# Kernel optimization log

Hardware: AMD Instinct MI355X
Metric: run time of the kernel (lower is better)

Reference implementation:

```python
import jax, jax.numpy as jnp
import numpy as np

D_MODEL = 1024
B, S = 4, 2048


def setup_inputs() -> dict:
    key = jax.random.key(0)
    kx, km, kq, kk, kv, ko = jax.random.split(key, 6)
    x = jax.random.normal(kx, (B, S, D_MODEL), dtype=jnp.float32)
    mask = jax.random.randint(km, (B, S, S), 0, 2).astype(jnp.bool_)
    # flax Dense default kernel init: lecun_normal-ish; plain scaled normal is fine for a reference
    init_scale = 1.0 / np.sqrt(D_MODEL)
    Wq = jax.random.normal(kq, (D_MODEL, D_MODEL), dtype=jnp.float32) * init_scale
    Wk = jax.random.normal(kk, (D_MODEL, D_MODEL), dtype=jnp.float32) * init_scale
    Wv = jax.random.normal(kv, (D_MODEL, D_MODEL), dtype=jnp.float32) * init_scale
    Wo = jax.random.normal(ko, (D_MODEL, D_MODEL), dtype=jnp.float32) * init_scale
    return {"x": x, "mask": mask, "Wq": Wq, "Wk": Wk, "Wv": Wv, "Wo": Wo}


def reference(x, mask, Wq, Wk, Wv, Wo):
    # QKV projections (use_bias=False)
    q = jnp.einsum('bsd,de->bse', x, Wq)
    k = jnp.einsum('bsd,de->bse', x, Wk)
    v = jnp.einsum('bsd,de->bse', x, Wv)
    scale = jnp.sqrt(jnp.asarray(q.shape[-1], x.dtype)).astype(x.dtype)
    # [B, S, S] attention scores
    attn_scores = jnp.einsum('bqd,bkd->bqk', q, k) / scale
    attn_scores = jnp.where(mask, attn_scores, jnp.asarray(-1e10, x.dtype))
    attn_weights = jax.nn.softmax(attn_scores, axis=-1)
    attn_output = jnp.einsum('bqk,bkd->bqd', attn_weights, v)
    return jnp.einsum('bsd,de->bse', attn_output, Wo)
```

## Files before the change

### kernel.cpp

```cpp
#include <hip/hip_runtime.h>


#define DM 1024
#define SQ 2048
#define NB 4
typedef unsigned short U16;
typedef short bhalf8 __attribute__((ext_vector_type(8)));
typedef float f32x4 __attribute__((ext_vector_type(4)));

__device__ inline U16 f2bf(float f) {
  unsigned int u = __float_as_uint(f);
  u += 0x7FFFu + ((u >> 16) & 1u);
  return (U16)(u >> 16);
}
__device__ inline float2 bfp2(unsigned int u) {
  float2 r;
  r.x = __uint_as_float(u << 16);
  r.y = __uint_as_float(u & 0xffff0000u);
  return r;
}
__device__ inline unsigned int packbf(float a, float b) {
  return (unsigned int)f2bf(a) | ((unsigned int)f2bf(b) << 16);
}

__device__ __forceinline__ void gload16(const U16* g, const U16* l) {
  unsigned int m0v =
      (unsigned int)__builtin_amdgcn_readfirstlane((int)(unsigned long long)l);
  asm volatile("s_mov_b32 m0, %0\n\t"
               "global_load_lds_dwordx4 %1, off"
               :
               : "s"(m0v), "v"(g)
               : "memory");
}

__global__ __launch_bounds__(256) void conv_f32_bf16(
    const float* __restrict__ src, U16* __restrict__ dst, float* __restrict__ rs) {
  int idx = blockIdx.x * 256 + threadIdx.x;
  if (idx < NB * SQ) rs[idx] = 0.f;
  int i = idx * 8;
  float4 a = *(const float4*)(src + i);
  float4 b = *(const float4*)(src + i + 4);
  uint4 w;
  w.x = packbf(a.x, a.y); w.y = packbf(a.z, a.w);
  w.z = packbf(b.x, b.y); w.w = packbf(b.z, b.w);
  *(uint4*)(dst + i) = w;
}

__device__ inline void ldcvt16(const float* p, U16* d) {
#pragma unroll
  for (int i = 0; i < 4; ++i) {
    float4 f = *(const float4*)(p + i * 4);
    d[i * 4 + 0] = f2bf(f.x); d[i * 4 + 1] = f2bf(f.y);
    d[i * 4 + 2] = f2bf(f.z); d[i * 4 + 3] = f2bf(f.w);
  }
}
__device__ inline void ldcvt16(const U16* p, U16* d) {
  uint4 a = *(const uint4*)p;
  uint4 b = *(const uint4*)(p + 8);
  *(uint4*)d = a;
  *(uint4*)(d + 8) = b;
}

__global__ __launch_bounds__(256) void transp_w4(
    const float* __restrict__ Wq, const float* __restrict__ Wk,
    const float* __restrict__ Wo, const float* __restrict__ Wv,
    U16* __restrict__ WT, U16* __restrict__ WoT, U16* __restrict__ Wv16) {
  __shared__ U16 tile[64][72];
  const int z = blockIdx.z;
  const int r0 = blockIdx.y * 64, c0 = blockIdx.x * 64;
  const int t = threadIdx.x;
  const int tr = t >> 2, tc = (t & 3) * 16;
  if (z == 3) {
    U16 vals[16];
    ldcvt16(Wv + (size_t)(r0 + tr) * DM + c0 + tc, vals);
    U16* op = Wv16 + (size_t)(r0 + tr) * DM + c0 + tc;
    *(uint4*)op = *(uint4*)&vals[0];
    *(uint4*)(op + 8) = *(uint4*)&vals[8];
    return;
  }
  const float* src = (z == 0) ? Wq : (z == 1) ? Wk : Wo;
  U16* d = (z == 2) ? WoT : WT + (size_t)z * DM * DM;
  ldcvt16(src + (size_t)(r0 + tr) * DM + c0 + tc, &tile[tr][tc]);
  __syncthreads();
  U16 vals[16];
#pragma unroll
  for (int m = 0; m < 16; ++m) vals[m] = tile[tc + m][tr];
  U16* op = d + (size_t)(c0 + tr) * DM + r0 + tc;
  *(uint4*)op = *(uint4*)&vals[0];
  *(uint4*)(op + 8) = *(uint4*)&vals[8];
}

__global__ __launch_bounds__(256) void transp_bf16(
    const U16* __restrict__ src, U16* __restrict__ dst, int R, int C) {
  __shared__ U16 tile[64][72];
  const int z = blockIdx.z;
  src += (size_t)z * R * C;
  dst += (size_t)z * R * C;
  const int r0 = blockIdx.y * 64, c0 = blockIdx.x * 64;
  const int t = threadIdx.x;
  const int tr = t >> 2, tc = (t & 3) * 16;
  ldcvt16(src + (size_t)(r0 + tr) * C + c0 + tc, &tile[tr][tc]);
  __syncthreads();
  U16 vals[16];
#pragma unroll
  for (int m = 0; m < 16; ++m) vals[m] = tile[tc + m][tr];
  U16* op = dst + (size_t)(c0 + tr) * R + r0 + tc;
  *(uint4*)op = *(uint4*)&vals[0];
  *(uint4*)(op + 8) = *(uint4*)&vals[8];
}

template <int EP>
__global__ __launch_bounds__(256) void gemm_mfma(
    const U16* __restrict__ A, const U16* __restrict__ B, void* __restrict__ Cv,
    int M, int N, int K, long long sA, long long sB, long long sC,
    const int* __restrict__ mask, float* __restrict__ rowsum, float scale) {
  __shared__ U16 As[128 * 72];
  __shared__ U16 Bs[128 * 72];
  const int t = threadIdx.x;
  const int lane = t & 63, wave = t >> 6;
  const int wm = wave >> 1, wn = wave & 1;
  const int q = lane >> 4, ln = lane & 15;
  const int z = blockIdx.z;
  const int m0 = blockIdx.y * 128, n0 = blockIdx.x * 128;
  A += (size_t)z * sA;
  B += (size_t)z * sB;

  f32x4 acc[4][4] = {};

  const int srow = t >> 3;
  const int scol = (t & 7) * 8;

  for (int k0 = 0; k0 < K; k0 += 64) {
    const U16* ga = A + (size_t)(m0 + srow) * K + k0 + scol;
    const U16* gb = B + (size_t)(n0 + srow) * K + k0 + scol;
#pragma unroll
    for (int it = 0; it < 4; ++it) {
      uint4 va = *(const uint4*)(ga + (size_t)it * 32 * K);
      uint4 vb = *(const uint4*)(gb + (size_t)it * 32 * K);
      *(uint4*)&As[(it * 32 + srow) * 72 + scol] = va;
      *(uint4*)&Bs[(it * 32 + srow) * 72 + scol] = vb;
    }
    __syncthreads();
#pragma unroll
    for (int kk = 0; kk < 64; kk += 32) {
      bhalf8 af[4], bg[4];
#pragma unroll
      for (int i = 0; i < 4; ++i) {
        af[i] = *(const bhalf8*)&As[(wm * 64 + i * 16 + ln) * 72 + kk + q * 8];
        bg[i] = *(const bhalf8*)&Bs[(wn * 64 + i * 16 + ln) * 72 + kk + q * 8];
      }
#pragma unroll
      for (int i = 0; i < 4; ++i)
#pragma unroll
        for (int j = 0; j < 4; ++j)
          acc[i][j] = __builtin_amdgcn_mfma_f32_16x16x32_bf16(af[i], bg[j], acc[i][j], 0, 0, 0);
    }
    __syncthreads();
  }

#pragma unroll
  for (int i = 0; i < 4; ++i) {
#pragma unroll
    for (int r = 0; r < 4; ++r) {
      const int rr = m0 + wm * 64 + i * 16 + q * 4 + r;
      float linv = 0.f;
      if constexpr (EP == 2) linv = 1.0f / (rowsum[(size_t)z * M + rr] + 1e-30f);
      float psum = 0.f;
#pragma unroll
      for (int j = 0; j < 4; ++j) {
        const int c = n0 + wn * 64 + j * 16 + ln;
        float v = acc[i][j][r];
        if constexpr (EP == 0) {
          ((U16*)Cv)[(size_t)z * sC + (size_t)rr * N + c] = f2bf(v);
        } else if constexpr (EP == 1) {
          int mk = mask[((size_t)z * M + rr) * N + c];
          float p = mk ? __expf(v * scale) : 0.f;
          U16 pb = f2bf(p);
          ((U16*)Cv)[(size_t)z * sC + (size_t)rr * N + c] = pb;
          psum += __uint_as_float((unsigned int)pb << 16);
        } else {
          ((float*)Cv)[(size_t)z * sC + (size_t)rr * N + c] = v * linv;
        }
      }
      if constexpr (EP == 1) {
#pragma unroll
        for (int off = 8; off > 0; off >>= 1) psum += __shfl_xor(psum, off, 64);
        if (ln == 0) atomicAdd(&rowsum[(size_t)z * M + rr], psum);
      }
    }
  }
}

template <int EP, int WM>
__global__ __launch_bounds__(512, 1) void gemm8(
    const U16* __restrict__ A, const U16* __restrict__ B, void* __restrict__ Cv,
    int M, int N, int K, long long sA, long long sB, long long sC,
    const int* __restrict__ mask, float* __restrict__ rowsum, float scale) {
  constexpr int WN = 8 / WM;
  constexpr int BN = WN * 64;
  constexpr int MR = 256 / WM;
  constexpr int FM = MR / 16;
  constexpr int IMq = FM / 2;
  constexpr int HB = BN / 2;
  constexpr int CB = HB / 64;
  constexpr int VW = 4 + 2 * CB;
  __shared__ __attribute__((aligned(16))) U16 Abuf[2][256 * 64];
  __shared__ __attribute__((aligned(16))) U16 Bbuf[2][BN * 64];
  const int t = threadIdx.x;
  const int lane = t & 63, wave = t >> 6;
  const int wm = wave / WN, wn = wave % WN;
  const int q = lane >> 4, ln = lane & 15;
  const int lxor = ln & 7;
  const int z = blockIdx.z;
  const int m0 = blockIdx.y * 256, n0 = blockIdx.x * BN;
  const U16* Abase = A + (size_t)z * sA + (size_t)m0 * K;
  const U16* Bbase = B + (size_t)z * sB + (size_t)n0 * K;

  const int pr = wave * 8 + (lane >> 3);
  const int cchunk = (((lane & 7) ^ ((lane >> 3) & 7)) << 3);
  int la[4];
#pragma unroll
  for (int c = 0; c < 4; ++c) {
    int p = c * 64 + pr;
    int mh = p >> 7, q64 = p & 127;
    la[c] = (q64 / (MR / 2)) * MR + mh * (MR / 2) + (q64 % (MR / 2));
  }
  int lb[4] = {0, 0, 0, 0};
#pragma unroll
  for (int c = 0; c < 2 * CB; ++c) {
    int p = c * 64 + pr;
    int nh = p / HB, rem = p % HB;
    lb[c] = (rem >> 5) * 64 + nh * 32 + (rem & 31);
  }
  const U16* gA0 = Abase + (size_t)la[0] * K + cchunk;
  const U16* gA1 = Abase + (size_t)la[1] * K + cchunk;
  const U16* gA2 = Abase + (size_t)la[2] * K + cchunk;
  const U16* gA3 = Abase + (size_t)la[3] * K + cchunk;
  const U16* gB0 = Bbase + (size_t)lb[0] * K + cchunk;
  const U16* gB1 = (CB == 2) ? Bbase + (size_t)lb[1] * K + cchunk : gB0;
  const U16* gB2 = Bbase + (size_t)lb[CB] * K + cchunk;
  const U16* gB3 = (CB == 2) ? Bbase + (size_t)lb[3] * K + cchunk : gB2;
  const int wofs = wave * 8 * 64;

#define ST_AX(bi, ko) { gload16(gA0 + (ko), &Abuf[bi][0 * 64 + wofs]);         \
                        gload16(gA1 + (ko), &Abuf[bi][64 * 64 + wofs]); }
#define ST_AY(bi, ko) { gload16(gA2 + (ko), &Abuf[bi][128 * 64 + wofs]);       \
                        gload16(gA3 + (ko), &Abuf[bi][192 * 64 + wofs]); }
#define ST_BE(bi, ko) { gload16(gB0 + (ko), &Bbuf[bi][0 * 64 + wofs]);         \
                        if (CB == 2) gload16(gB1 + (ko), &Bbuf[bi][64 * 64 + wofs]); }
#define ST_BO(bi, ko) { gload16(gB2 + (ko), &Bbuf[bi][HB * 64 + wofs]);        \
                        if (CB == 2) gload16(gB3 + (ko), &Bbuf[bi][(HB + 64) * 64 + wofs]); }

  f32x4 acc[FM][4] = {};
  bhalf8 af[IMq][2], bgE[2][2], bgO[2][2];

#define LDA(bi, mh) {                                                          \
  _Pragma("unroll") for (int im = 0; im < IMq; ++im)                           \
  _Pragma("unroll") for (int kx = 0; kx < 2; ++kx)                             \
    af[im][kx] = *(const bhalf8*)&Abuf[bi][                                    \
        ((mh) * 128 + wm * (MR / 2) + im * 16 + ln) * 64 +                     \
        (((kx * 4 + q) ^ lxor) << 3)]; }
#define LDB(bi, nh, BG) {                                                      \
  _Pragma("unroll") for (int jn = 0; jn < 2; ++jn)                             \
  _Pragma("unroll") for (int kx = 0; kx < 2; ++kx)                             \
    BG[jn][kx] = *(const bhalf8*)&Bbuf[bi][                                    \
        ((nh) * HB + wn * 32 + jn * 16 + ln) * 64 +                            \
        (((kx * 4 + q) ^ lxor) << 3)]; }
#define MQ(mh, nh, BG) {                                                       \
  __builtin_amdgcn_s_setprio(1);                                               \
  _Pragma("unroll") for (int im = 0; im < IMq; ++im)                           \
  _Pragma("unroll") for (int jn = 0; jn < 2; ++jn)                             \
  _Pragma("unroll") for (int kx = 0; kx < 2; ++kx)                             \
    acc[(mh) * IMq + im][(nh) * 2 + jn] =                                      \
        __builtin_amdgcn_mfma_f32_16x16x32_bf16(                               \
            af[im][kx], BG[jn][kx], acc[(mh) * IMq + im][(nh) * 2 + jn],       \
            0, 0, 0);                                                          \
  __builtin_amdgcn_s_setprio(0); }
#define WAITV(n) asm volatile("s_waitcnt vmcnt(%0)" :: "i"(n) : "memory")
#define BAR() __builtin_amdgcn_s_barrier()
#define LGKM0() asm volatile("s_waitcnt lgkmcnt(0)" ::: "memory")

#define TILE8(bi, nbi, kA, kB)                                                 \
  {                                                                            \
    ST_BO(nbi, kA); WAITV(VW);                                                 \
    LDA(bi, 0); LDB(bi, 0, bgE);                                               \
    BAR(); LGKM0(); MQ(0, 0, bgE); BAR();                                      \
    ST_AY(nbi, kA); WAITV(VW);                                                 \
    LDB(bi, 1, bgO);                                                           \
    BAR(); LGKM0(); MQ(0, 1, bgO); BAR();                                      \
    ST_AX(bi, kB); WAITV(VW);                                                  \
    LDA(bi, 1);                                                                \
    BAR(); LGKM0(); MQ(1, 0, bgE); BAR();                                      \
    ST_BE(bi, kB); WAITV(VW);                                                  \
    BAR(); LGKM0(); MQ(1, 1, bgO); BAR();                                      \
  }

  const int NT = K >> 6;
  ST_AX(0, 0); ST_BE(0, 0); ST_BO(0, 0); ST_AY(0, 0);
  ST_AX(1, 64); ST_BE(1, 64);
  WAITV(VW); BAR();
  for (int tt = 0; tt < NT; tt += 2) {
    const int k1 = (tt + 1) * 64;
    const int k2 = (tt + 2 < NT) ? (tt + 2) * 64 : 0;
    const int k3 = (tt + 3 < NT) ? (tt + 3) * 64 : 0;
    TILE8(0, 1, k1, k2);
    TILE8(1, 0, k2, k3);
  }
  WAITV(0);

#undef ST_AX
#undef ST_AY
#undef ST_BE
#undef ST_BO
#undef LDA
#undef LDB
#undef MQ
#undef WAITV
#undef BAR
#undef LGKM0
#undef TILE8

#pragma unroll
  for (int i = 0; i < FM; ++i) {
#pragma unroll
    for (int r = 0; r < 4; ++r) {
      const int rr = m0 + wm * MR + i * 16 + q * 4 + r;
      float linv = 0.f;
      if constexpr (EP == 2) linv = 1.0f / (rowsum[(size_t)z * M + rr] + 1e-30f);
      float psum = 0.f;
#pragma unroll
      for (int j = 0; j < 4; ++j) {
        const int c = n0 + wn * 64 + j * 16 + ln;
        float v = acc[i][j][r];
        if constexpr (EP == 0) {
          ((U16*)Cv)[(size_t)z * sC + (size_t)rr * N + c] = f2bf(v);
        } else if constexpr (EP == 1) {
          int mk = mask[((size_t)z * M + rr) * N + c];
          float p = mk ? __expf(v * scale) : 0.f;
          U16 pb = f2bf(p);
          ((U16*)Cv)[(size_t)z * sC + (size_t)rr * N + c] = pb;
          psum += __uint_as_float((unsigned int)pb << 16);
        } else {
          ((float*)Cv)[(size_t)z * sC + (size_t)rr * N + c] = v * linv;
        }
      }
      if constexpr (EP == 1) {
#pragma unroll
        for (int off = 8; off > 0; off >>= 1) psum += __shfl_xor(psum, off, 64);
        if (ln == 0) atomicAdd(&rowsum[(size_t)z * M + rr], psum);
      }
    }
  }
}

__device__ inline float4 load4(const float* p) { return *(const float4*)p; }
__device__ inline float4 load4(const U16* p) {
  uint2 w = *(const uint2*)p;
  float2 f0 = bfp2(w.x), f1 = bfp2(w.y);
  return make_float4(f0.x, f0.y, f1.x, f1.y);
}
__device__ inline void store4(float* p, float a, float b, float c, float d) {
  *(float4*)p = make_float4(a, b, c, d);
}
__device__ inline void store4(U16* p, float a, float b, float c, float d) {
  uint2 w;
  w.x = packbf(a, b);
  w.y = packbf(c, d);
  *(uint2*)p = w;
}
template <typename TA, typename TB, typename TC>
__global__ __launch_bounds__(256) void gemm_t(
    const TA* __restrict__ A, const TB* __restrict__ B,
    TC* __restrict__ C, int M, int N, int K) {
  __shared__ float As[16][64];
  __shared__ float Bs[16][64];
  const int t = threadIdx.x;
  const int tx = t & 15, ty = t >> 4;
  const int m0 = blockIdx.y * 64;
  const int n0 = blockIdx.x * 64;
  const int arow = t >> 2, akq = (t & 3) * 4;
  const int brow = t >> 4, bcg = (t & 15) * 4;
  float acc[4][4] = {};
  for (int k0 = 0; k0 < K; k0 += 16) {
    {
      float4 f = load4(A + (size_t)(m0 + arow) * K + k0 + akq);
      As[akq + 0][arow] = f.x; As[akq + 1][arow] = f.y;
      As[akq + 2][arow] = f.z; As[akq + 3][arow] = f.w;
    }
    {
      float4 f = load4(B + (size_t)(k0 + brow) * N + n0 + bcg);
      *(float4*)&Bs[brow][bcg] = f;
    }
    __syncthreads();
#pragma unroll
    for (int kk = 0; kk < 16; ++kk) {
      float4 a = *(const float4*)&As[kk][ty * 4];
      float4 b = *(const float4*)&Bs[kk][tx * 4];
      float av[4] = {a.x, a.y, a.z, a.w};
      float bv[4] = {b.x, b.y, b.z, b.w};
#pragma unroll
      for (int i = 0; i < 4; ++i)
#pragma unroll
        for (int j = 0; j < 4; ++j) acc[i][j] += av[i] * bv[j];
    }
    __syncthreads();
  }
#pragma unroll
  for (int i = 0; i < 4; ++i)
    store4(&C[(size_t)(m0 + ty * 4 + i) * N + n0 + tx * 4],
           acc[i][0], acc[i][1], acc[i][2], acc[i][3]);
}
__global__ __launch_bounds__(256) void flash_wave(
    const U16* __restrict__ Q, const U16* __restrict__ Kd,
    const U16* __restrict__ V, const int* __restrict__ mask,
    U16* __restrict__ O) {
  __shared__ float q_s[4][DM];
  const int t = threadIdx.x;
  const int w = t >> 6;
  const int lane = t & 63;
  const int row = blockIdx.x * 4 + w;
  const int b = row >> 11;
  const size_t bo = (size_t)b * SQ * DM;
  const size_t mrow0 = (size_t)row * SQ;
  {
    const U16* qp = Q + (size_t)row * DM + lane * 16;
    uint4 w0 = *(const uint4*)qp;
    uint4 w1 = *(const uint4*)(qp + 8);
    float* dst = &q_s[w][lane * 16];
    float2 f;
    f = bfp2(w0.x); dst[0] = f.x;  dst[1] = f.y;
    f = bfp2(w0.y); dst[2] = f.x;  dst[3] = f.y;
    f = bfp2(w0.z); dst[4] = f.x;  dst[5] = f.y;
    f = bfp2(w0.w); dst[6] = f.x;  dst[7] = f.y;
    f = bfp2(w1.x); dst[8] = f.x;  dst[9] = f.y;
    f = bfp2(w1.y); dst[10] = f.x; dst[11] = f.y;
    f = bfp2(w1.z); dst[12] = f.x; dst[13] = f.y;
    f = bfp2(w1.w); dst[14] = f.x; dst[15] = f.y;
  }
  __syncthreads();
  float m = -3.0e38f, l = 0.f;
  float o[16] = {};
  const int dbase = lane * 16;
  const float* qrow = q_s[w];
  for (int j0 = 0; j0 < SQ; j0 += 64) {
    float s;
    {
      const U16* kp = Kd + bo + (size_t)(j0 + lane) * DM;
      float acc = 0.f;
      for (int d = 0; d < DM; d += 8) {
        uint4 kw = *(const uint4*)(kp + d);
        float2 a0 = bfp2(kw.x), a1 = bfp2(kw.y), a2 = bfp2(kw.z), a3 = bfp2(kw.w);
        acc += qrow[d] * a0.x + qrow[d + 1] * a0.y + qrow[d + 2] * a1.x +
               qrow[d + 3] * a1.y + qrow[d + 4] * a2.x + qrow[d + 5] * a2.y +
               qrow[d + 6] * a3.x + qrow[d + 7] * a3.y;
      }
      s = acc * 0.03125f;
      if (mask[mrow0 + j0 + lane] == 0) s = -1e10f;
    }
    float ms = s;
#pragma unroll
    for (int off = 32; off > 0; off >>= 1) ms = fmaxf(ms, __shfl_xor(ms, off, 64));
    float mn = fmaxf(m, ms);
    float alpha = __expf(m - mn);
    float p = __expf(s - mn);
    float ps = p;
#pragma unroll
    for (int off = 32; off > 0; off >>= 1) ps += __shfl_xor(ps, off, 64);
    l = l * alpha + ps;
    m = mn;
#pragma unroll
    for (int k = 0; k < 16; ++k) o[k] *= alpha;
    const U16* vp = V + bo + (size_t)j0 * DM + dbase;
    for (int j = 0; j < 64; ++j) {
      float pj = __shfl(p, j, 64);
      uint4 v0 = *(const uint4*)(vp + (size_t)j * DM);
      uint4 v1 = *(const uint4*)(vp + (size_t)j * DM + 8);
      float2 f0 = bfp2(v0.x), f1 = bfp2(v0.y), f2 = bfp2(v0.z), f3 = bfp2(v0.w);
      float2 g0 = bfp2(v1.x), g1 = bfp2(v1.y), g2 = bfp2(v1.z), g3 = bfp2(v1.w);
      o[0] += pj * f0.x;  o[1] += pj * f0.y;  o[2] += pj * f1.x;  o[3] += pj * f1.y;
      o[4] += pj * f2.x;  o[5] += pj * f2.y;  o[6] += pj * f3.x;  o[7] += pj * f3.y;
      o[8] += pj * g0.x;  o[9] += pj * g0.y;  o[10] += pj * g1.x; o[11] += pj * g1.y;
      o[12] += pj * g2.x; o[13] += pj * g2.y; o[14] += pj * g3.x; o[15] += pj * g3.y;
    }
  }
  float linv = (l > 0.f) ? (1.0f / l) : 0.f;
  U16* op = O + (size_t)row * DM + dbase;
  uint4 r0, r1;
  r0.x = packbf(o[0] * linv, o[1] * linv);
  r0.y = packbf(o[2] * linv, o[3] * linv);
  r0.z = packbf(o[4] * linv, o[5] * linv);
  r0.w = packbf(o[6] * linv, o[7] * linv);
  r1.x = packbf(o[8] * linv, o[9] * linv);
  r1.y = packbf(o[10] * linv, o[11] * linv);
  r1.z = packbf(o[12] * linv, o[13] * linv);
  r1.w = packbf(o[14] * linv, o[15] * linv);
  *(uint4*)op = r0;
  *(uint4*)(op + 8) = r1;
}

extern "C" void kernel_launch(void* const* d_in, const int* in_sizes, int n_in,
                              void* d_out, int out_size, void* d_ws, size_t ws_size,
                              hipStream_t stream) {
  const float* x  = (const float*)d_in[0];
  const int* mask = (const int*)d_in[1];
  const float* Wq = (const float*)d_in[2];
  const float* Wk = (const float*)d_in[3];
  const float* Wv = (const float*)d_in[4];
  const float* Wo = (const float*)d_in[5];
  float* out = (float*)d_out;

  const size_t MB = 1u << 20;
  const size_t E = (size_t)NB * SQ * DM;
  const size_t WE = (size_t)DM * DM;

  if (ws_size >= 121 * MB) {
    char* ws = (char*)d_ws;
    U16* WT   = (U16*)ws;
    U16* WoT  = (U16*)(ws + 6 * MB);
    U16* x16  = (U16*)(ws + 8 * MB);
    U16* Q16  = (U16*)(ws + 24 * MB);
    U16* K16  = (U16*)(ws + 40 * MB);
    U16* U16b = (U16*)(ws + 56 * MB);
    U16* Wv16 = (U16*)(ws + 72 * MB);
    U16* UT16 = (U16*)(ws + 72 * MB);
    U16* P16  = (U16*)(ws + 88 * MB);
    float* rs = (float*)(ws + 120 * MB);

    conv_f32_bf16<<<dim3(E / (256 * 8)), 256, 0, stream>>>(x, x16, rs);
    transp_w4<<<dim3(16, 16, 4), 256, 0, stream>>>(Wq, Wk, Wo, Wv, WT, WoT, Wv16);

    gemm_mfma<0><<<dim3(DM / 128, DM / 128, 1), 256, 0, stream>>>(
        WoT, Wv16, WT + 2 * WE, DM, DM, DM, 0, 0, 0, nullptr, nullptr, 0.f);

    gemm8<0, 4><<<dim3(DM / 128, (NB * SQ) / 256, 3), 512, 0, stream>>>(
        x16, WT, Q16, NB * SQ, DM, DM,
        0, (long long)WE, (long long)E, nullptr, nullptr, 0.f);

    transp_bf16<<<dim3(DM / 64, SQ / 64, NB), 256, 0, stream>>>(U16b, UT16, SQ, DM);

    gemm8<1, 2><<<dim3(SQ / 256, SQ / 256, NB), 512, 0, stream>>>(
        Q16, K16, P16, SQ, SQ, DM,
        (long long)SQ * DM, (long long)SQ * DM, (long long)SQ * SQ,
        mask, rs, 0.03125f);

    gemm8<2, 4><<<dim3(DM / 128, SQ / 256, NB), 512, 0, stream>>>(
        P16, UT16, out, SQ, DM, SQ,
        (long long)SQ * SQ, (long long)DM * SQ, (long long)SQ * DM,
        nullptr, rs, 0.f);
  } else {
    U16* Kw = (U16*)d_ws;
    U16* Vw = Kw + E;
    U16* Qw = Vw + E;
    U16* Ow = Qw;
    dim3 blk(256);
    dim3 gg(DM / 64, (NB * SQ) / 64);
    gemm_t<float, float, U16><<<gg, blk, 0, stream>>>(x, Wk, Kw, NB * SQ, DM, DM);
    gemm_t<float, float, U16><<<gg, blk, 0, stream>>>(x, Wv, Vw, NB * SQ, DM, DM);
    gemm_t<float, float, U16><<<gg, blk, 0, stream>>>(x, Wq, Qw, NB * SQ, DM, DM);
    flash_wave<<<dim3((NB * SQ) / 4), blk, 0, stream>>>(Qw, Kw, Vw, mask, Ow);
    gemm_t<U16, float, float><<<gg, blk, 0, stream>>>(Ow, Wo, out, NB * SQ, DM, DM);
  }
}
```

Before: 339.6 us.

## Remap blocks across XCDs and restructure GEMM k-loop to cut barriers

Block indices are remapped so that consecutive logical tiles are spread round-robin across the eight XCDs, which is meant to improve L2 locality of shared A/B panels. The per-tile pipeline is rewritten to use two A fragment register sets (afX/afY), so LDS reads for the second half can be issued earlier and the number of barriers and vmcnt waits per K-step drops. The cost is more VGPR pressure from the extra fragment buffers. There is also a risk of LDS races from the looser synchronisation, and the remap assumes the total block count is divisible by 8.

```diff
diff --git a/kernel.cpp b/kernel.cpp
--- a/kernel.cpp
+++ b/kernel.cpp
@@ -203,7 +203,8 @@
   constexpr int IMq = FM / 2;
   constexpr int HB = BN / 2;
   constexpr int CB = HB / 64;
-  constexpr int VW = 4 + 2 * CB;
+  constexpr int VW1 = 2 + 2 * CB;
+  constexpr int VW2 = 4 + 2 * CB;
   __shared__ __attribute__((aligned(16))) U16 Abuf[2][256 * 64];
   __shared__ __attribute__((aligned(16))) U16 Bbuf[2][BN * 64];
   const int t = threadIdx.x;
@@ -211,10 +212,18 @@
   const int wm = wave / WN, wn = wave % WN;
   const int q = lane >> 4, ln = lane & 15;
   const int lxor = ln & 7;
-  const int z = blockIdx.z;
-  const int m0 = blockIdx.y * 256, n0 = blockIdx.x * BN;
-  const U16* Abase = A + (size_t)z * sA + (size_t)m0 * K;
-  const U16* Bbase = B + (size_t)z * sB + (size_t)n0 * K;
+
+  const int gx = gridDim.x, gy = gridDim.y;
+  int lin = blockIdx.x + gx * (blockIdx.y + gy * blockIdx.z);
+  const int cpx = (gx * gy * gridDim.z) >> 3;
+  lin = (lin & 7) * cpx + (lin >> 3);
+  const int bz = lin / (gx * gy);
+  const int rem = lin - bz * gx * gy;
+  const int by = rem / gx, bx = rem - by * gx;
+
+  const int m0 = by * 256, n0 = bx * BN;
+  const U16* Abase = A + (size_t)bz * sA + (size_t)m0 * K;
+  const U16* Bbase = B + (size_t)bz * sB + (size_t)n0 * K;
 
   const int pr = wave * 8 + (lane >> 3);
   const int cchunk = (((lane & 7) ^ ((lane >> 3) & 7)) << 3);
@@ -229,8 +238,8 @@
 #pragma unroll
   for (int c = 0; c < 2 * CB; ++c) {
     int p = c * 64 + pr;
-    int nh = p / HB, rem = p % HB;
-    lb[c] = (rem >> 5) * 64 + nh * 32 + (rem & 31);
+    int nh = p / HB, rem2 = p % HB;
+    lb[c] = (rem2 >> 5) * 64 + nh * 32 + (rem2 & 31);
   }
   const U16* gA0 = Abase + (size_t)la[0] * K + cchunk;
   const U16* gA1 = Abase + (size_t)la[1] * K + cchunk;
@@ -252,59 +261,61 @@
                         if (CB == 2) gload16(gB3 + (ko), &Bbuf[bi][(HB + 64) * 64 + wofs]); }
 
   f32x4 acc[FM][4] = {};
-  bhalf8 af[IMq][2], bgE[2][2], bgO[2][2];
-
-#define LDA(bi, mh) {                                                          \
+  bhalf8 afX[IMq][2], afY[IMq][2], bgE[2][2], bgO[2][2];
+
+#define LDA(bi, mh, DST) {                                                     \
   _Pragma("unroll") for (int im = 0; im < IMq; ++im)                           \
   _Pragma("unroll") for (int kx = 0; kx < 2; ++kx)                             \
-    af[im][kx] = *(const bhalf8*)&Abuf[bi][                                    \
+    DST[im][kx] = *(const bhalf8*)&Abuf[bi][                                   \
         ((mh) * 128 + wm * (MR / 2) + im * 16 + ln) * 64 +                     \
         (((kx * 4 + q) ^ lxor) << 3)]; }
-#define LDB(bi, nh, BG) {                                                      \
+#define LDB(bi, nh, DST) {                                                     \
   _Pragma("unroll") for (int jn = 0; jn < 2; ++jn)                             \
   _Pragma("unroll") for (int kx = 0; kx < 2; ++kx)                             \
-    BG[jn][kx] = *(const bhalf8*)&Bbuf[bi][                                    \
+    DST[jn][kx] = *(const bhalf8*)&Bbuf[bi][                                   \
         ((nh) * HB + wn * 32 + jn * 16 + ln) * 64 +                            \
         (((kx * 4 + q) ^ lxor) << 3)]; }
-#define MQ(mh, nh, BG) {                                                       \
+#define MQ(mh, nh, AF, BG) {                                                   \
   __builtin_amdgcn_s_setprio(1);                                               \
   _Pragma("unroll") for (int im = 0; im < IMq; ++im)                           \
   _Pragma("unroll") for (int jn = 0; jn < 2; ++jn)                             \
   _Pragma("unroll") for (int kx = 0; kx < 2; ++kx)                             \
     acc[(mh) * IMq + im][(nh) * 2 + jn] =                                      \
         __builtin_amdgcn_mfma_f32_16x16x32_bf16(                               \
-            af[im][kx], BG[jn][kx], acc[(mh) * IMq + im][(nh) * 2 + jn],       \
+            AF[im][kx], BG[jn][kx], acc[(mh) * IMq + im][(nh) * 2 + jn],       \
             0, 0, 0);                                                          \
   __builtin_amdgcn_s_setprio(0); }
 #define WAITV(n) asm volatile("s_waitcnt vmcnt(%0)" :: "i"(n) : "memory")
 #define BAR() __builtin_amdgcn_s_barrier()
 #define LGKM0() asm volatile("s_waitcnt lgkmcnt(0)" ::: "memory")
 
-#define TILE8(bi, nbi, kA, kB)                                                 \
+#define TILE(bi, nbi, kA, kB)                                                  \
   {                                                                            \
-    ST_BO(nbi, kA); WAITV(VW);                                                 \
-    LDA(bi, 0); LDB(bi, 0, bgE);                                               \
-    BAR(); LGKM0(); MQ(0, 0, bgE); BAR();                                      \
-    ST_AY(nbi, kA); WAITV(VW);                                                 \
-    LDB(bi, 1, bgO);                                                           \
-    BAR(); LGKM0(); MQ(0, 1, bgO); BAR();                                      \
-    ST_AX(bi, kB); WAITV(VW);                                                  \
-    LDA(bi, 1);                                                                \
-    BAR(); LGKM0(); MQ(1, 0, bgE); BAR();                                      \
-    ST_BE(bi, kB); WAITV(VW);                                                  \
-    BAR(); LGKM0(); MQ(1, 1, bgO); BAR();                                      \
+    LDA(bi, 0, afX); LDB(bi, 0, bgE);                                          \
+    ST_BO(nbi, kA);                                                            \
+    WAITV(VW1); BAR(); LGKM0();                                                \
+    MQ(0, 0, afX, bgE);                                                        \
+    LDA(bi, 1, afY); LDB(bi, 1, bgO);                                          \
+    ST_AY(nbi, kA);                                                            \
+    BAR(); LGKM0();                                                            \
+    MQ(0, 1, afX, bgO);                                                        \
+    ST_AX(bi, kB);                                                             \
+    MQ(1, 0, afY, bgE);                                                        \
+    ST_BE(bi, kB);                                                             \
+    WAITV(VW2); BAR();                                                         \
+    MQ(1, 1, afY, bgO);                                                        \
   }
 
   const int NT = K >> 6;
   ST_AX(0, 0); ST_BE(0, 0); ST_BO(0, 0); ST_AY(0, 0);
   ST_AX(1, 64); ST_BE(1, 64);
-  WAITV(VW); BAR();
+  WAITV(VW2); BAR();
   for (int tt = 0; tt < NT; tt += 2) {
     const int k1 = (tt + 1) * 64;
     const int k2 = (tt + 2 < NT) ? (tt + 2) * 64 : 0;
     const int k3 = (tt + 3 < NT) ? (tt + 3) * 64 : 0;
-    TILE8(0, 1, k1, k2);
-    TILE8(1, 0, k2, k3);
+    TILE(0, 1, k1, k2);
+    TILE(1, 0, k2, k3);
   }
   WAITV(0);
 
@@ -318,7 +329,7 @@
 #undef WAITV
 #undef BAR
 #undef LGKM0
-#undef TILE8
+#undef TILE
 
 #pragma unroll
   for (int i = 0; i < FM; ++i) {
@@ -326,28 +337,28 @@
     for (int r = 0; r < 4; ++r) {
       const int rr = m0 + wm * MR + i * 16 + q * 4 + r;
       float linv = 0.f;
-      if constexpr (EP == 2) linv = 1.0f / (rowsum[(size_t)z * M + rr] + 1e-30f);
+      if constexpr (EP == 2) linv = 1.0f / (rowsum[(size_t)bz * M + rr] + 1e-30f);
       float psum = 0.f;
 #pragma unroll
       for (int j = 0; j < 4; ++j) {
         const int c = n0 + wn * 64 + j * 16 + ln;
         float v = acc[i][j][r];
         if constexpr (EP == 0) {
-          ((U16*)Cv)[(size_t)z * sC + (size_t)rr * N + c] = f2bf(v);
+          ((U16*)Cv)[(size_t)bz * sC + (size_t)rr * N + c] = f2bf(v);
         } else if constexpr (EP == 1) {
-          int mk = mask[((size_t)z * M + rr) * N + c];
+          int mk = mask[((size_t)bz * M + rr) * N + c];
           float p = mk ? __expf(v * scale) : 0.f;
           U16 pb = f2bf(p);
-          ((U16*)Cv)[(size_t)z * sC + (size_t)rr * N + c] = pb;
+          ((U16*)Cv)[(size_t)bz * sC + (size_t)rr * N + c] = pb;
           psum += __uint_as_float((unsigned int)pb << 16);
         } else {
-          ((float*)Cv)[(size_t)z * sC + (size_t)rr * N + c] = v * linv;
+          ((float*)Cv)[(size_t)bz * sC + (size_t)rr * N + c] = v * linv;
         }
       }
       if constexpr (EP == 1) {
 #pragma unroll
         for (int off = 8; off > 0; off >>= 1) psum += __shfl_xor(psum, off, 64);
-        if (ln == 0) atomicAdd(&rowsum[(size_t)z * M + rr], psum);
+        if (ln == 0) atomicAdd(&rowsum[(size_t)bz * M + rr], psum);
       }
     }
   }
```

After: 331.7 us. 1.02x faster.

## Pack attention mask into bitmasks and remap gemm8 block order

Applied to the files above, without the earlier changes.

Adds a pre-pass that turns the int32 mask into 64-bit ballot bitmasks, so the score GEMM epilogue reads one U64 per row segment instead of 64 ints. This cuts mask traffic in the softmax-fused epilogue at the cost of an extra pass over the mask. It also remaps gemm8 block indices so consecutive linear block IDs spread in strides of eight, apparently to spread work across XCDs for better L2 locality. It drops the unused mask path from gemm_mfma's epilogue.

```diff
diff --git a/kernel.cpp b/kernel.cpp
--- a/kernel.cpp
+++ b/kernel.cpp
@@ -5,6 +5,7 @@
 #define SQ 2048
 #define NB 4
 typedef unsigned short U16;
+typedef unsigned long long U64;
 typedef short bhalf8 __attribute__((ext_vector_type(8)));
 typedef float f32x4 __attribute__((ext_vector_type(4)));
 
@@ -44,6 +45,19 @@
   w.x = packbf(a.x, a.y); w.y = packbf(a.z, a.w);
   w.z = packbf(b.x, b.y); w.w = packbf(b.z, b.w);
   *(uint4*)(dst + i) = w;
+}
+
+__global__ __launch_bounds__(256) void pack_mask(
+    const int* __restrict__ mask, U64* __restrict__ pm) {
+  const int lane = threadIdx.x & 63;
+  const int wv = (blockIdx.x * 256 + threadIdx.x) >> 6;
+#pragma unroll 4
+  for (int i = 0; i < 32; ++i) {
+    size_t g = (size_t)wv * 32 + i;
+    int mk = mask[g * 64 + lane];
+    U64 b = __ballot(mk != 0);
+    if (lane == 0) pm[g] = b;
+  }
 }
 
 __device__ inline void ldcvt16(const float* p, U16* d) {
@@ -165,28 +179,16 @@
       const int rr = m0 + wm * 64 + i * 16 + q * 4 + r;
       float linv = 0.f;
       if constexpr (EP == 2) linv = 1.0f / (rowsum[(size_t)z * M + rr] + 1e-30f);
-      float psum = 0.f;
 #pragma unroll
       for (int j = 0; j < 4; ++j) {
         const int c = n0 + wn * 64 + j * 16 + ln;
         float v = acc[i][j][r];
         if constexpr (EP == 0) {
           ((U16*)Cv)[(size_t)z * sC + (size_t)rr * N + c] = f2bf(v);
-        } else if constexpr (EP == 1) {
-          int mk = mask[((size_t)z * M + rr) * N + c];
-          float p = mk ? __expf(v * scale) : 0.f;
-          U16 pb = f2bf(p);
-          ((U16*)Cv)[(size_t)z * sC + (size_t)rr * N + c] = pb;
-          psum += __uint_as_float((unsigned int)pb << 16);
         } else {
           ((float*)Cv)[(size_t)z * sC + (size_t)rr * N + c] = v * linv;
         }
       }
-      if constexpr (EP == 1) {
-#pragma unroll
-        for (int off = 8; off > 0; off >>= 1) psum += __shfl_xor(psum, off, 64);
-        if (ln == 0) atomicAdd(&rowsum[(size_t)z * M + rr], psum);
-      }
     }
   }
 }
@@ -195,7 +197,7 @@
 __global__ __launch_bounds__(512, 1) void gemm8(
     const U16* __restrict__ A, const U16* __restrict__ B, void* __restrict__ Cv,
     int M, int N, int K, long long sA, long long sB, long long sC,
-    const int* __restrict__ mask, float* __restrict__ rowsum, float scale) {
+    const U64* __restrict__ pmask, float* __restrict__ rowsum, float scale) {
   constexpr int WN = 8 / WM;
   constexpr int BN = WN * 64;
   constexpr int MR = 256 / WM;
@@ -211,10 +213,18 @@
   const int wm = wave / WN, wn = wave % WN;
   const int q = lane >> 4, ln = lane & 15;
   const int lxor = ln & 7;
-  const int z = blockIdx.z;
-  const int m0 = blockIdx.y * 256, n0 = blockIdx.x * BN;
-  const U16* Abase = A + (size_t)z * sA + (size_t)m0 * K;
-  const U16* Bbase = B + (size_t)z * sB + (size_t)n0 * K;
+
+  const int gx = gridDim.x, gy = gridDim.y;
+  int lin = blockIdx.x + gx * (blockIdx.y + gy * blockIdx.z);
+  const int cpx = (gx * gy * gridDim.z) >> 3;
+  lin = (lin & 7) * cpx + (lin >> 3);
+  const int bz = lin / (gx * gy);
+  const int rem = lin - bz * gx * gy;
+  const int by = rem / gx, bx = rem - by * gx;
+
+  const int m0 = by * 256, n0 = bx * BN;
+  const U16* Abase = A + (size_t)bz * sA + (size_t)m0 * K;
+  const U16* Bbase = B + (size_t)bz * sB + (size_t)n0 * K;
 
   const int pr = wave * 8 + (lane >> 3);
   const int cchunk = (((lane & 7) ^ ((lane >> 3) & 7)) << 3);
@@ -229,8 +239,8 @@
 #pragma unroll
   for (int c = 0; c < 2 * CB; ++c) {
     int p = c * 64 + pr;
-    int nh = p / HB, rem = p % HB;
-    lb[c] = (rem >> 5) * 64 + nh * 32 + (rem & 31);
+    int nh = p / HB, rem2 = p % HB;
+    lb[c] = (rem2 >> 5) * 64 + nh * 32 + (rem2 & 31);
   }
   const U16* gA0 = Abase + (size_t)la[0] * K + cchunk;
   const U16* gA1 = Abase + (size_t)la[1] * K + cchunk;
@@ -326,28 +336,31 @@
     for (int r = 0; r < 4; ++r) {
       const int rr = m0 + wm * MR + i * 16 + q * 4 + r;
       float linv = 0.f;
-      if constexpr (EP == 2) linv = 1.0f / (rowsum[(size_t)z * M + rr] + 1e-30f);
+      if constexpr (EP == 2) linv = 1.0f / (rowsum[(size_t)bz * M + rr] + 1e-30f);
+      U64 m64 = 0;
+      if constexpr (EP == 1)
+        m64 = pmask[((size_t)bz * M + rr) * (N >> 6) + (n0 >> 6) + wn];
       float psum = 0.f;
 #pragma unroll
       for (int j = 0; j < 4; ++j) {
         const int c = n0 + wn * 64 + j * 16 + ln;
         float v = acc[i][j][r];
         if constexpr (EP == 0) {
-          ((U16*)Cv)[(size_t)z * sC + (size_t)rr * N + c] = f2bf(v);
+          ((U16*)Cv)[(size_t)bz * sC + (size_t)rr * N + c] = f2bf(v);
         } else if constexpr (EP == 1) {
-          int mk = mask[((size_t)z * M + rr) * N + c];
+          int mk = (int)((m64 >> (j * 16 + ln)) & 1ull);
           float p = mk ? __expf(v * scale) : 0.f;
           U16 pb = f2bf(p);
-          ((U16*)Cv)[(size_t)z * sC + (size_t)rr * N + c] = pb;
+          ((U16*)Cv)[(size_t)bz * sC + (size_t)rr * N + c] = pb;
           psum += __uint_as_float((unsigned int)pb << 16);
         } else {
-          ((float*)Cv)[(size_t)z * sC + (size_t)rr * N + c] = v * linv;
+          ((float*)Cv)[(size_t)bz * sC + (size_t)rr * N + c] = v * linv;
         }
       }
       if constexpr (EP == 1) {
 #pragma unroll
         for (int off = 8; off > 0; off >>= 1) psum += __shfl_xor(psum, off, 64);
-        if (ln == 0) atomicAdd(&rowsum[(size_t)z * M + rr], psum);
+        if (ln == 0) atomicAdd(&rowsum[(size_t)bz * M + rr], psum);
       }
     }
   }
@@ -517,6 +530,7 @@
     char* ws = (char*)d_ws;
     U16* WT   = (U16*)ws;
     U16* WoT  = (U16*)(ws + 6 * MB);
+    U64* pm   = (U64*)(ws + 6 * MB);
     U16* x16  = (U16*)(ws + 8 * MB);
     U16* Q16  = (U16*)(ws + 24 * MB);
     U16* K16  = (U16*)(ws + 40 * MB);
@@ -532,6 +546,8 @@
     gemm_mfma<0><<<dim3(DM / 128, DM / 128, 1), 256, 0, stream>>>(
         WoT, Wv16, WT + 2 * WE, DM, DM, DM, 0, 0, 0, nullptr, nullptr, 0.f);
 
+    pack_mask<<<dim3(2048), 256, 0, stream>>>(mask, pm);
+
     gemm8<0, 4><<<dim3(DM / 128, (NB * SQ) / 256, 3), 512, 0, stream>>>(
         x16, WT, Q16, NB * SQ, DM, DM,
         0, (long long)WE, (long long)E, nullptr, nullptr, 0.f);
@@ -541,7 +557,7 @@
     gemm8<1, 2><<<dim3(SQ / 256, SQ / 256, NB), 512, 0, stream>>>(
         Q16, K16, P16, SQ, SQ, DM,
         (long long)SQ * DM, (long long)SQ * DM, (long long)SQ * SQ,
-        mask, rs, 0.03125f);
+        pm, rs, 0.03125f);
 
     gemm8<2, 4><<<dim3(DM / 128, SQ / 256, NB), 512, 0, stream>>>(
         P16, UT16, out, SQ, DM, SQ,
```

Measured after the change: 324.3 us. 4.5% less time.
